# Kernel optimization log

Hardware: AMD Instinct MI355X
Metric: run time of the kernel (lower is better)

## Reference

```python
import jax, jax.numpy as jnp
import numpy as np

FILTERS = 128
DN = ('NHWC', 'HWIO', 'NHWC')
T1 = 1.0
RTOL = 1e-3
ATOL = 1e-3
DT0 = 0.05
MAX_STEPS = 32  # upper bound on adaptive solver steps (dopri5 at rtol=1e-3 uses far fewer)


def _conv(x, w):
    return jax.lax.conv_general_dilated(x, w, (1, 1), 'SAME', dimension_numbers=DN)


def _ode_func(y, t, w1, b1, w2, b2):
    # f(y, t) = relu(conv(relu(conv([y, t], w1)+b1) ++ t, w2)+b2), time appended as extra channel
    def cat_t(x):
        return jnp.concatenate([x, jnp.ones(x.shape[:-1] + (1,), x.dtype) * t], axis=-1)
    h = jax.nn.relu(_conv(cat_t(y), w1) + b1)
    return jax.nn.relu(_conv(cat_t(h), w2) + b2)


def _dopri5(y0, w1, b1, w2, b2):
    # Adaptive Dormand-Prince RK45 from t=0 to t=1, matching tf.contrib.integrate.odeint defaults
    f = lambda y, t: _ode_func(y, t, w1, b1, w2, b2)

    def rk_step(y, t, dt):
        k1 = f(y, t)
        k2 = f(y + dt * (0.2 * k1), t + 0.2 * dt)
        k3 = f(y + dt * (3. / 40 * k1 + 9. / 40 * k2), t + 0.3 * dt)
        k4 = f(y + dt * (44. / 45 * k1 - 56. / 15 * k2 + 32. / 9 * k3), t + 0.8 * dt)
        k5 = f(y + dt * (19372. / 6561 * k1 - 25360. / 2187 * k2 + 64448. / 6561 * k3
                         - 212. / 729 * k4), t + 8. / 9 * dt)
        k6 = f(y + dt * (9017. / 3168 * k1 - 355. / 33 * k2 + 46732. / 5247 * k3
                         + 49. / 176 * k4 - 5103. / 18656 * k5), t + dt)
        y5 = y + dt * (35. / 384 * k1 + 500. / 1113 * k3 + 125. / 192 * k4
                       - 2187. / 6784 * k5 + 11. / 84 * k6)
        k7 = f(y5, t + dt)  # FSAL stage, used only for the error estimate here
        err = dt * ((35. / 384 - 5179. / 57600) * k1 + (500. / 1113 - 7571. / 16695) * k3
                    + (125. / 192 - 393. / 640) * k4 + (-2187. / 6784 + 92097. / 339200) * k5
                    + (11. / 84 - 187. / 2100) * k6 - (1. / 40) * k7)
        return y5, err

    def step(carry, _):
        y, t, dt, done = carry
        dt_c = jnp.minimum(dt, T1 - t)  # never overshoot t1
        y_new, err = rk_step(y, t, dt_c)
        scale = ATOL + RTOL * jnp.maximum(jnp.abs(y), jnp.abs(y_new))
        err_norm = jnp.sqrt(jnp.mean(jnp.square(err / scale)))
        err_norm = jax.lax.stop_gradient(jnp.maximum(err_norm, 1e-10))
        accept = err_norm <= 1.0
        factor = jnp.clip(0.9 * err_norm ** -0.2, 0.2, 10.0)
        adv = accept & jnp.logical_not(done)
        y = jnp.where(adv, y_new, y)
        t = jnp.where(adv, t + dt_c, t)
        dt = jnp.where(done, dt, dt_c * factor)
        done = done | (t >= T1 - 1e-6)
        return (y, t, dt, done), None

    init = (y0, jnp.float32(0.0), jnp.float32(DT0), jnp.array(False))
    (y, _, _, _), _ = jax.lax.scan(jax.checkpoint(step), init, None, length=MAX_STEPS)
    return y


def setup_inputs() -> dict:
    key = jax.random.key(0)
    k0, k1, k2 = jax.random.split(key, 3)
    B, H, W, F = 32, 32, 32, FILTERS
    kh = kw = 3
    # glorot_uniform for HWIO conv kernel: fan_in = kh*kw*(F+1), fan_out = kh*kw*F
    lim = float(np.sqrt(6.0 / (kh * kw * (F + 1) + kh * kw * F)))
    x = jax.random.normal(k0, (B, H, W, F), jnp.float32)
    w1 = jax.random.uniform(k1, (kh, kw, F + 1, F), jnp.float32, -lim, lim)
    w2 = jax.random.uniform(k2, (kh, kw, F + 1, F), jnp.float32, -lim, lim)
    b1 = jnp.zeros((F,), jnp.float32)
    b2 = jnp.zeros((F,), jnp.float32)
    return {"x": x, "w1": w1, "b1": b1, "w2": w2, "b2": b2}


def reference(x, w1, b1, w2, b2):
    return _dopri5(x, w1, b1, w2, b2)
```

## Files before the change

kernel.cpp:

```cpp
#include <hip/hip_runtime.h>
#include <math.h>

#define NB    32
#define NHW   32
#define NC    128
#define NTOT  (NB*NHW*NHW*NC)
#define N4    (NTOT/4)
#define N8    (NTOT/8)
#define KDIM  1152

typedef unsigned short u16;
typedef __attribute__((ext_vector_type(8))) short short8v;
typedef __attribute__((ext_vector_type(4))) float float4v;

__device__ inline float b2f(u16 u) { union { unsigned int i; float f; } x; x.i = ((unsigned int)u) << 16; return x.f; }
__device__ inline u16   f2b(float f) {
    union { unsigned int i; float f; } x; x.f = f;
    unsigned int u = x.i;
    return (u16)((u + 0x7fffu + ((u >> 16) & 1u)) >> 16);
}
__device__ inline void ld8(const u16* __restrict__ p, float* v) {
    uint4 r = *(const uint4*)p;
    v[0] = b2f((u16)(r.x & 0xffff)); v[1] = b2f((u16)(r.x >> 16));
    v[2] = b2f((u16)(r.y & 0xffff)); v[3] = b2f((u16)(r.y >> 16));
    v[4] = b2f((u16)(r.z & 0xffff)); v[5] = b2f((u16)(r.z >> 16));
    v[6] = b2f((u16)(r.w & 0xffff)); v[7] = b2f((u16)(r.w >> 16));
}
__device__ inline uint4 pk8(const float* v) {
    uint4 o;
    o.x = (unsigned int)f2b(v[0]) | ((unsigned int)f2b(v[1]) << 16);
    o.y = (unsigned int)f2b(v[2]) | ((unsigned int)f2b(v[3]) << 16);
    o.z = (unsigned int)f2b(v[4]) | ((unsigned int)f2b(v[5]) << 16);
    o.w = (unsigned int)f2b(v[6]) | ((unsigned int)f2b(v[7]) << 16);
    return o;
}
__device__ inline void fma8(float* __restrict__ v, const u16* __restrict__ p, float s) {
    float kv[8];
    ld8(p, kv);
    #pragma unroll
    for (int j = 0; j < 8; ++j) v[j] = fmaf(s, kv[j], v[j]);
}


__global__ __launch_bounds__(64) void init_kernel(float* __restrict__ st, double* __restrict__ acc)
{
    int i = threadIdx.x;
    if (i < 32) acc[i] = 0.0;
    if (i == 0) { st[0]=0.0f; st[1]=0.05f; st[2]=0.05f; st[3]=0.0f; st[4]=0.0f; }
}

__global__ __launch_bounds__(256) void prep_kernel(
    const float* __restrict__ w, short* __restrict__ Wt, float* __restrict__ Et)
{
    const int part = blockIdx.x;
    const int tid = threadIdx.x;
    if (part < 9) {
        const int tap = part;
        for (int i = tid; i < 128*128; i += 256) {
            const int ci = i >> 7, co = i & 127;
            Wt[co*KDIM + tap*128 + ci] = (short)f2b(w[(tap*129 + ci)*128 + co]);
        }
    } else {
        for (int i = tid; i < 9*128; i += 256) {
            const int cls = i >> 7, co = i & 127;
            const int cy = cls / 3, cx = cls % 3;
            float s = 0.f;
            for (int ky = 0; ky < 3; ++ky) {
                if ((cy==0 && ky==0) || (cy==2 && ky==2)) continue;
                for (int kx = 0; kx < 3; ++kx) {
                    if ((cx==0 && kx==0) || (cx==2 && kx==2)) continue;
                    s += w[((ky*3+kx)*129 + 128)*128 + co];
                }
            }
            Et[cls*128 + co] = s;
        }
    }
}

__global__ __launch_bounds__(256) void copy_kernel(float* __restrict__ dst, const float* __restrict__ src)
{
    int stride = gridDim.x * blockDim.x;
    for (int i = blockIdx.x*blockDim.x + threadIdx.x; i < N4; i += stride)
        reinterpret_cast<float4*>(dst)[i] = reinterpret_cast<const float4*>(src)[i];
}

__global__ __launch_bounds__(256) void copy_if_adv_kernel(float* __restrict__ dst,
                                                          const float* __restrict__ src,
                                                          const float* __restrict__ st)
{
    if (st[4] == 0.0f) return;
    int stride = gridDim.x * blockDim.x;
    for (int i = blockIdx.x*blockDim.x + threadIdx.x; i < N4; i += stride)
        reinterpret_cast<float4*>(dst)[i] = reinterpret_cast<const float4*>(src)[i];
}

template<int NK>
__global__ __launch_bounds__(256) void conv_mfma(
    const float* __restrict__ basef, const u16* __restrict__ bfin,
    const u16* __restrict__ ka, const u16* __restrict__ kb,
    const u16* __restrict__ kc, const u16* __restrict__ kd,
    const u16* __restrict__ ke,
    float ca, float cb, float cc2, float cd, float ce,
    const short* __restrict__ Wt, const float* __restrict__ bias,
    const float* __restrict__ Et,
    u16* __restrict__ out,
    const float* __restrict__ st, float cfrac)
{
    if (st[3] != 0.0f) return;
    __shared__ __align__(16) char lds[180*256];
    const int b    = blockIdx.y;
    const int tile = blockIdx.x;
    const int ty   = (tile >> 2) * 16;
    const int tx   = (tile & 3) * 8;
    const int tid  = threadIdx.x;
    const float dt = st[2];

    const size_t ibase = (size_t)b * (NHW*NHW*NC);
    for (int i = tid; i < 180*16; i += 256) {
        const int pos = i >> 4, cc = i & 15;
        const int sy = pos / 10, sx = pos - sy*10;
        const int gy = ty + sy - 1, gx = tx + sx - 1;
        const bool ok = ((unsigned)gy < 32u) && ((unsigned)gx < 32u);
        uint4 w128;
        if (!ok) {
            w128 = make_uint4(0u, 0u, 0u, 0u);
        } else if (NK < 0) {
            w128 = *(const uint4*)(bfin + ibase + (size_t)(gy*32 + gx)*128 + cc*8);
        } else {
            const size_t idx = ibase + (size_t)(gy*32 + gx)*128 + cc*8;
            float v[8];
            *(float4*)(v)     = *(const float4*)(basef + idx);
            *(float4*)(v + 4) = *(const float4*)(basef + idx + 4);
            if (NK >= 1) fma8(v, ka + idx, dt*ca);
            if (NK >= 2) fma8(v, kb + idx, dt*cb);
            if (NK >= 3) fma8(v, kc + idx, dt*cc2);
            if (NK >= 4) fma8(v, kd + idx, dt*cd);
            if (NK >= 5) fma8(v, ke + idx, dt*ce);
            w128 = pk8(v);
        }
        *(uint4*)(lds + pos*256 + ((cc*16) ^ ((pos & 7) << 4))) = w128;
    }
    __syncthreads();

    const int l  = tid & 63;
    const int w  = tid >> 6;
    const int wy = w >> 1, wx = w & 1;
    const int lr = l & 15,  kg = l >> 4;

    float4v acc[4][4];
    #pragma unroll
    for (int ra = 0; ra < 4; ++ra)
        #pragma unroll
        for (int nb = 0; nb < 4; ++nb)
            acc[ra][nb] = (float4v){0.f, 0.f, 0.f, 0.f};

    int sy0[4], sx0[4];
    #pragma unroll
    for (int ra = 0; ra < 4; ++ra) {
        const int r = wy*64 + ra*16 + lr;
        sy0[ra] = r >> 3; sx0[ra] = r & 7;
    }

    #pragma unroll
    for (int ky = 0; ky < 3; ++ky) {
        #pragma unroll
        for (int kx = 0; kx < 3; ++kx) {
            const int tap = ky*3 + kx;
            #pragma unroll
            for (int kk = 0; kk < 4; ++kk) {
                short8v a[4], bb[4];
                const int cc = kk*4 + kg;
                #pragma unroll
                for (int ra = 0; ra < 4; ++ra) {
                    const int pos = (sy0[ra] + ky)*10 + sx0[ra] + kx;
                    a[ra] = *(const short8v*)(lds + pos*256 + ((cc*16) ^ ((pos & 7) << 4)));
                }
                const short* wb = Wt + tap*128 + kk*32 + kg*8;
                #pragma unroll
                for (int nb = 0; nb < 4; ++nb) {
                    const int cout = wx*64 + nb*16 + lr;
                    bb[nb] = *(const short8v*)(wb + (size_t)cout*KDIM);
                }
                #pragma unroll
                for (int ra = 0; ra < 4; ++ra)
                    #pragma unroll
                    for (int nb = 0; nb < 4; ++nb)
                        acc[ra][nb] = __builtin_amdgcn_mfma_f32_16x16x32_bf16(a[ra], bb[nb], acc[ra][nb], 0, 0, 0);
            }
        }
    }

    const float tval = st[0] + cfrac*dt;
    #pragma unroll
    for (int nb = 0; nb < 4; ++nb) {
        const int cout = wx*64 + nb*16 + lr;
        const float bsv = bias[cout];
        #pragma unroll
        for (int ra = 0; ra < 4; ++ra) {
            #pragma unroll
            for (int ri = 0; ri < 4; ++ri) {
                const int r  = wy*64 + ra*16 + kg*4 + ri;
                const int yy = ty + (r >> 3), xx = tx + (r & 7);
                const int cy = (yy == 0) ? 0 : ((yy == 31) ? 2 : 1);
                const int cx = (xx == 0) ? 0 : ((xx == 31) ? 2 : 1);
                float v = acc[ra][nb][ri] + bsv + tval*Et[(cy*3 + cx)*128 + cout];
                v = fmaxf(v, 0.f);
                out[(size_t)b*131072 + (size_t)(yy*32 + xx)*128 + cout] = f2b(v);
            }
        }
    }
}

__global__ __launch_bounds__(256) void axpy5_kernel(
    float* __restrict__ y5, const float* __restrict__ y,
    const u16* __restrict__ k1, const u16* __restrict__ k3,
    const u16* __restrict__ k4, const u16* __restrict__ k5,
    const u16* __restrict__ k6,
    float c1, float c3, float c4, float c5, float c6,
    const float* __restrict__ st)
{
    if (st[3] != 0.0f) return;
    const float dt = st[2];
    int stride = gridDim.x * blockDim.x;
    for (int i = blockIdx.x*blockDim.x + threadIdx.x; i < N8; i += stride) {
        const size_t base = (size_t)i * 8;
        float v[8];
        *(float4*)(v)     = *(const float4*)(y + base);
        *(float4*)(v + 4) = *(const float4*)(y + base + 4);
        fma8(v, k1 + base, dt*c1);
        fma8(v, k3 + base, dt*c3);
        fma8(v, k4 + base, dt*c4);
        fma8(v, k5 + base, dt*c5);
        fma8(v, k6 + base, dt*c6);
        *(float4*)(y5 + base)     = *(const float4*)(v);
        *(float4*)(y5 + base + 4) = *(const float4*)(v + 4);
    }
}

__global__ __launch_bounds__(256) void err_reduce_kernel(
    const float* __restrict__ y,  const float* __restrict__ y5,
    const u16* __restrict__ k1, const u16* __restrict__ k3,
    const u16* __restrict__ k4, const u16* __restrict__ k5,
    const u16* __restrict__ k6, const u16* __restrict__ k7,
    const float* __restrict__ st, double* __restrict__ acc_slot)
{
    if (st[3] != 0.0f) return;
    const float dt = st[2];
    const float E1 = (float)(35.0/384.0 - 5179.0/57600.0);
    const float E3 = (float)(500.0/1113.0 - 7571.0/16695.0);
    const float E4 = (float)(125.0/192.0 - 393.0/640.0);
    const float E5 = (float)(-2187.0/6784.0 + 92097.0/339200.0);
    const float E6 = (float)(11.0/84.0 - 187.0/2100.0);
    const float E7 = (float)(-1.0/40.0);
    float lsum = 0.f;
    int stride = gridDim.x*blockDim.x;
    for (int i = blockIdx.x*blockDim.x + threadIdx.x; i < N8; i += stride) {
        const size_t base = (size_t)i * 8;
        float a[8], c[8], d[8], e[8], f[8], g[8], yv[8], v5[8];
        ld8(k1 + base, a); ld8(k3 + base, c); ld8(k4 + base, d);
        ld8(k5 + base, e); ld8(k6 + base, f); ld8(k7 + base, g);
        *(float4*)(yv)     = *(const float4*)(y + base);
        *(float4*)(yv + 4) = *(const float4*)(y + base + 4);
        *(float4*)(v5)     = *(const float4*)(y5 + base);
        *(float4*)(v5 + 4) = *(const float4*)(y5 + base + 4);
        #pragma unroll
        for (int j = 0; j < 8; ++j) {
            float err = dt*(E1*a[j] + E3*c[j] + E4*d[j] + E5*e[j] + E6*f[j] + E7*g[j]);
            float sc  = 1e-3f + 1e-3f*fmaxf(fabsf(yv[j]), fabsf(v5[j]));
            float r = err/sc; lsum += r*r;
        }
    }
    #pragma unroll
    for (int off = 32; off > 0; off >>= 1) lsum += __shfl_down(lsum, off, 64);
    __shared__ float ws_[4];
    int wid = threadIdx.x >> 6, lane = threadIdx.x & 63;
    if (lane == 0) ws_[wid] = lsum;
    __syncthreads();
    if (threadIdx.x == 0) {
        float bs = ws_[0] + ws_[1] + ws_[2] + ws_[3];
        atomicAdd(acc_slot, (double)bs);
    }
}

__global__ __launch_bounds__(64) void ctrl_kernel(float* __restrict__ st, const double* __restrict__ acc_slot)
{
    if (threadIdx.x != 0) return;
    float t = st[0], dt = st[1], dtc = st[2];
    bool done = (st[3] != 0.0f);
    float err_norm = sqrtf((float)(*acc_slot / (double)NTOT));
    err_norm = fmaxf(err_norm, 1e-10f);
    bool accept = (err_norm <= 1.0f);
    float factor = 0.9f * powf(err_norm, -0.2f);
    factor = fminf(fmaxf(factor, 0.2f), 10.0f);
    bool adv = accept && !done;
    if (adv) t = t + dtc;
    if (!done) dt = dtc * factor;
    done = done || (t >= 1.0f - 1e-6f);
    st[0] = t; st[1] = dt; st[3] = done ? 1.0f : 0.0f; st[4] = adv ? 1.0f : 0.0f;
    st[2] = fminf(dt, 1.0f - t);
}

extern "C" void kernel_launch(void* const* d_in, const int* in_sizes, int n_in,
                              void* d_out, int out_size, void* d_ws, size_t ws_size,
                              hipStream_t stream)
{
    const float* x  = (const float*)d_in[0];
    const float* w1 = (const float*)d_in[1];
    const float* b1 = (const float*)d_in[2];
    const float* w2 = (const float*)d_in[3];
    const float* b2 = (const float*)d_in[4];

    char* ws = (char*)d_ws;
    double* acc = (double*)ws;
    float*  st  = (float*)(ws + 256);
    float*  E1t = (float*)(ws + 512);
    float*  E2t = (float*)(ws + 5120);
    short*  Wt1 = (short*)(ws + 10240);
    short*  Wt2 = (short*)(ws + 10240 + 294912);
    char*   bufs = ws + 1048576;
    float* y  = (float*)(bufs);
    float* y5 = (float*)(bufs + (size_t)NTOT*4);
    u16*   h  = (u16*)(bufs + (size_t)NTOT*8);
    u16*   k1 = (u16*)(bufs + (size_t)NTOT*10);
    u16*   k2 = (u16*)(bufs + (size_t)NTOT*12);
    u16*   k3 = (u16*)(bufs + (size_t)NTOT*14);
    u16*   k4 = (u16*)(bufs + (size_t)NTOT*16);
    u16*   k5 = (u16*)(bufs + (size_t)NTOT*18);
    u16*   k6 = (u16*)(bufs + (size_t)NTOT*20);
    u16*   k7 = (u16*)(bufs + (size_t)NTOT*22);

    const dim3 cgrid(8, NB);
    const dim3 cblk(256);
    const int ab = 2048;

    const float A21 = 0.2f;
    const float A31 = (float)(3.0/40.0),      A32 = (float)(9.0/40.0);
    const float A41 = (float)(44.0/45.0),     A42 = (float)(-56.0/15.0),     A43 = (float)(32.0/9.0);
    const float A51 = (float)(19372.0/6561.0),A52 = (float)(-25360.0/2187.0),A53 = (float)(64448.0/6561.0), A54 = (float)(-212.0/729.0);
    const float A61 = (float)(9017.0/3168.0), A62 = (float)(-355.0/33.0),    A63 = (float)(46732.0/5247.0), A64 = (float)(49.0/176.0), A65 = (float)(-5103.0/18656.0);
    const float B1  = (float)(35.0/384.0),    B3  = (float)(500.0/1113.0),   B4  = (float)(125.0/192.0),    B5  = (float)(-2187.0/6784.0), B6 = (float)(11.0/84.0);
    const float C2 = 0.2f, C3 = 0.3f, C4 = 0.8f, C5 = (float)(8.0/9.0);

    init_kernel<<<1, 64, 0, stream>>>(st, acc);
    prep_kernel<<<10, 256, 0, stream>>>(w1, Wt1, E1t);
    prep_kernel<<<10, 256, 0, stream>>>(w2, Wt2, E2t);
    copy_kernel<<<ab, 256, 0, stream>>>(y, x);

    for (int it = 0; it < 32; ++it) {
        conv_mfma<0><<<cgrid, cblk, 0, stream>>>(y, h, k1,k1,k1,k1,k1, 0,0,0,0,0, Wt1, b1, E1t, h,  st, 0.0f);
        conv_mfma<-1><<<cgrid, cblk, 0, stream>>>(y, h, k1,k1,k1,k1,k1, 0,0,0,0,0, Wt2, b2, E2t, k1, st, 0.0f);
        conv_mfma<1><<<cgrid, cblk, 0, stream>>>(y, h, k1,k1,k1,k1,k1, A21,0,0,0,0, Wt1, b1, E1t, h,  st, C2);
        conv_mfma<-1><<<cgrid, cblk, 0, stream>>>(y, h, k1,k1,k1,k1,k1, 0,0,0,0,0, Wt2, b2, E2t, k2, st, C2);
        conv_mfma<2><<<cgrid, cblk, 0, stream>>>(y, h, k1,k2,k1,k1,k1, A31,A32,0,0,0, Wt1, b1, E1t, h,  st, C3);
        conv_mfma<-1><<<cgrid, cblk, 0, stream>>>(y, h, k1,k1,k1,k1,k1, 0,0,0,0,0, Wt2, b2, E2t, k3, st, C3);
        conv_mfma<3><<<cgrid, cblk, 0, stream>>>(y, h, k1,k2,k3,k1,k1, A41,A42,A43,0,0, Wt1, b1, E1t, h,  st, C4);
        conv_mfma<-1><<<cgrid, cblk, 0, stream>>>(y, h, k1,k1,k1,k1,k1, 0,0,0,0,0, Wt2, b2, E2t, k4, st, C4);
        conv_mfma<4><<<cgrid, cblk, 0, stream>>>(y, h, k1,k2,k3,k4,k1, A51,A52,A53,A54,0, Wt1, b1, E1t, h,  st, C5);
        conv_mfma<-1><<<cgrid, cblk, 0, stream>>>(y, h, k1,k1,k1,k1,k1, 0,0,0,0,0, Wt2, b2, E2t, k5, st, C5);
        conv_mfma<5><<<cgrid, cblk, 0, stream>>>(y, h, k1,k2,k3,k4,k5, A61,A62,A63,A64,A65, Wt1, b1, E1t, h,  st, 1.0f);
        conv_mfma<-1><<<cgrid, cblk, 0, stream>>>(y, h, k1,k1,k1,k1,k1, 0,0,0,0,0, Wt2, b2, E2t, k6, st, 1.0f);
        axpy5_kernel<<<ab, 256, 0, stream>>>(y5, y, k1, k3, k4, k5, k6, B1, B3, B4, B5, B6, st);
        conv_mfma<0><<<cgrid, cblk, 0, stream>>>(y5, h, k1,k1,k1,k1,k1, 0,0,0,0,0, Wt1, b1, E1t, h,  st, 1.0f);
        conv_mfma<-1><<<cgrid, cblk, 0, stream>>>(y5, h, k1,k1,k1,k1,k1, 0,0,0,0,0, Wt2, b2, E2t, k7, st, 1.0f);
        err_reduce_kernel<<<ab, 256, 0, stream>>>(y, y5, k1, k3, k4, k5, k6, k7, st, acc + it);
        ctrl_kernel<<<1, 64, 0, stream>>>(st, acc + it);
        copy_if_adv_kernel<<<ab, 256, 0, stream>>>(y, y5, st);
    }

    copy_kernel<<<ab, 256, 0, stream>>>((float*)d_out, y);

    (void)in_sizes; (void)n_in; (void)out_size; (void)ws_size;
}
```

Baseline: 3.021 ms.

## Fuse both convolutions per stage with halo recompute and ping-pong state buffers

Each ODE function evaluation now runs in one kernel: the first conv is computed on a 10x10 halo region into LDS, then the second conv reads it directly, so the bf16 intermediate h no longer goes through global memory. The y5 combination is folded into the stage-7 evaluation, the error reduction and step control are merged using a last-block atomic counter, and y/y5 swap roles via a flag instead of a conditional copy. The cost is redundant halo computation in the first conv (100 positions computed for 64 outputs), 8x8 tiles with more blocks, and fewer kernel launches per step.

```diff
diff --git a/kernel.cpp b/kernel.cpp
--- a/kernel.cpp
+++ b/kernel.cpp
@@ -1,13 +1,11 @@
 #include <hip/hip_runtime.h>
 #include <math.h>
 
-#define NB    32
-#define NHW   32
-#define NC    128
-#define NTOT  (NB*NHW*NHW*NC)
-#define N4    (NTOT/4)
-#define N8    (NTOT/8)
+#define NTOT  4194304
+#define N4    1048576
+#define N8    524288
 #define KDIM  1152
+#define EGRID 512
 
 typedef unsigned short u16;
 typedef __attribute__((ext_vector_type(8))) short short8v;
@@ -41,12 +39,22 @@
     for (int j = 0; j < 8; ++j) v[j] = fmaf(s, kv[j], v[j]);
 }
 
-
-__global__ __launch_bounds__(64) void init_kernel(float* __restrict__ st, double* __restrict__ acc)
+constexpr float A21 = 0.2f;
+constexpr float A31 = (float)(3.0/40.0),       A32 = (float)(9.0/40.0);
+constexpr float A41 = (float)(44.0/45.0),      A42 = (float)(-56.0/15.0),      A43 = (float)(32.0/9.0);
+constexpr float A51 = (float)(19372.0/6561.0), A52 = (float)(-25360.0/2187.0), A53 = (float)(64448.0/6561.0), A54 = (float)(-212.0/729.0);
+constexpr float A61 = (float)(9017.0/3168.0),  A62 = (float)(-355.0/33.0),     A63 = (float)(46732.0/5247.0), A64 = (float)(49.0/176.0), A65 = (float)(-5103.0/18656.0);
+constexpr float B1c = (float)(35.0/384.0),     B3c = (float)(500.0/1113.0),    B4c = (float)(125.0/192.0),    B5c = (float)(-2187.0/6784.0), B6c = (float)(11.0/84.0);
+constexpr float CF2 = 0.2f, CF3 = 0.3f, CF4 = 0.8f, CF5 = (float)(8.0/9.0);
+
+
+__global__ __launch_bounds__(64) void init_kernel(float* __restrict__ st,
+                                                  double* __restrict__ acc,
+                                                  unsigned* __restrict__ cnt)
 {
     int i = threadIdx.x;
-    if (i < 32) acc[i] = 0.0;
-    if (i == 0) { st[0]=0.0f; st[1]=0.05f; st[2]=0.05f; st[3]=0.0f; st[4]=0.0f; }
+    if (i < 32) { acc[i] = 0.0; cnt[i] = 0u; }
+    if (i == 0) { st[0]=0.0f; st[1]=0.05f; st[2]=0.05f; st[3]=0.0f; st[4]=0.0f; st[5]=0.0f; }
 }
 
 __global__ __launch_bounds__(256) void prep_kernel(
@@ -77,183 +85,213 @@
     }
 }
 
-__global__ __launch_bounds__(256) void copy_kernel(float* __restrict__ dst, const float* __restrict__ src)
+__global__ __launch_bounds__(256) void copy_in_kernel(float* __restrict__ dst, const float* __restrict__ src)
 {
     int stride = gridDim.x * blockDim.x;
     for (int i = blockIdx.x*blockDim.x + threadIdx.x; i < N4; i += stride)
         reinterpret_cast<float4*>(dst)[i] = reinterpret_cast<const float4*>(src)[i];
 }
 
-__global__ __launch_bounds__(256) void copy_if_adv_kernel(float* __restrict__ dst,
-                                                          const float* __restrict__ src,
-                                                          const float* __restrict__ st)
-{
-    if (st[4] == 0.0f) return;
+__global__ __launch_bounds__(256) void copy_out_kernel(float* __restrict__ dst,
+                                                       const float* __restrict__ yA,
+                                                       const float* __restrict__ yB,
+                                                       const float* __restrict__ st)
+{
+    const float* y = (st[5] != 0.0f) ? yB : yA;
     int stride = gridDim.x * blockDim.x;
     for (int i = blockIdx.x*blockDim.x + threadIdx.x; i < N4; i += stride)
-        reinterpret_cast<float4*>(dst)[i] = reinterpret_cast<const float4*>(src)[i];
-}
-
-template<int NK>
-__global__ __launch_bounds__(256) void conv_mfma(
-    const float* __restrict__ basef, const u16* __restrict__ bfin,
+        reinterpret_cast<float4*>(dst)[i] = reinterpret_cast<const float4*>(y)[i];
+}
+
+template<int NK, bool STY5>
+__global__ __launch_bounds__(256) void feval_kernel(
+    const float* __restrict__ yAp, float* __restrict__ yBp,
     const u16* __restrict__ ka, const u16* __restrict__ kb,
     const u16* __restrict__ kc, const u16* __restrict__ kd,
     const u16* __restrict__ ke,
-    float ca, float cb, float cc2, float cd, float ce,
-    const short* __restrict__ Wt, const float* __restrict__ bias,
-    const float* __restrict__ Et,
-    u16* __restrict__ out,
+    float ca, float cb, float cc, float cd, float ce,
+    const short* __restrict__ Wt1, const float* __restrict__ b1g, const float* __restrict__ E1g,
+    const short* __restrict__ Wt2, const float* __restrict__ b2g, const float* __restrict__ E2g,
+    u16* __restrict__ kout,
     const float* __restrict__ st, float cfrac)
 {
     if (st[3] != 0.0f) return;
-    __shared__ __align__(16) char lds[180*256];
-    const int b    = blockIdx.y;
+    __shared__ __align__(16) char ldsA[144*256];
+    __shared__ __align__(16) char ldsH[100*256];
+
+    const int flag = (st[5] != 0.0f);
+    const float* yb  = flag ? (const float*)yBp : yAp;
+    float*       y5b = flag ? (float*)yAp : yBp;
+
+    const int img  = blockIdx.y;
     const int tile = blockIdx.x;
-    const int ty   = (tile >> 2) * 16;
+    const int ty   = ((tile >> 2) & 3) * 8;
     const int tx   = (tile & 3) * 8;
     const int tid  = threadIdx.x;
-    const float dt = st[2];
-
-    const size_t ibase = (size_t)b * (NHW*NHW*NC);
-    for (int i = tid; i < 180*16; i += 256) {
-        const int pos = i >> 4, cc = i & 15;
-        const int sy = pos / 10, sx = pos - sy*10;
-        const int gy = ty + sy - 1, gx = tx + sx - 1;
-        const bool ok = ((unsigned)gy < 32u) && ((unsigned)gx < 32u);
-        uint4 w128;
-        if (!ok) {
-            w128 = make_uint4(0u, 0u, 0u, 0u);
-        } else if (NK < 0) {
-            w128 = *(const uint4*)(bfin + ibase + (size_t)(gy*32 + gx)*128 + cc*8);
-        } else {
-            const size_t idx = ibase + (size_t)(gy*32 + gx)*128 + cc*8;
-            float v[8];
-            *(float4*)(v)     = *(const float4*)(basef + idx);
-            *(float4*)(v + 4) = *(const float4*)(basef + idx + 4);
-            if (NK >= 1) fma8(v, ka + idx, dt*ca);
-            if (NK >= 2) fma8(v, kb + idx, dt*cb);
-            if (NK >= 3) fma8(v, kc + idx, dt*cc2);
-            if (NK >= 4) fma8(v, kd + idx, dt*cd);
-            if (NK >= 5) fma8(v, ke + idx, dt*ce);
-            w128 = pk8(v);
-        }
-        *(uint4*)(lds + pos*256 + ((cc*16) ^ ((pos & 7) << 4))) = w128;
+    const float dt   = st[2];
+    const float tval = st[0] + cfrac * dt;
+    const size_t ibase = (size_t)img * 131072;
+
+    {
+        const float s1 = dt*ca, s2 = dt*cb, s3 = dt*cc, s4 = dt*cd, s5 = dt*ce;
+        for (int i = tid; i < 144*16; i += 256) {
+            const int pos = i >> 4, ch8 = i & 15;
+            const int iy = pos / 12, ix = pos - iy*12;
+            const int gy = ty + iy - 2, gx = tx + ix - 2;
+            uint4 w128 = make_uint4(0u, 0u, 0u, 0u);
+            if ((unsigned)gy < 32u && (unsigned)gx < 32u) {
+                const size_t idx = ibase + (size_t)((gy << 5) + gx)*128 + ch8*8;
+                float v[8];
+                *(float4*)(v)     = *(const float4*)(yb + idx);
+                *(float4*)(v + 4) = *(const float4*)(yb + idx + 4);
+                if (NK >= 1) fma8(v, ka + idx, s1);
+                if (NK >= 2) fma8(v, kb + idx, s2);
+                if (NK >= 3) fma8(v, kc + idx, s3);
+                if (NK >= 4) fma8(v, kd + idx, s4);
+                if (NK >= 5) fma8(v, ke + idx, s5);
+                if (STY5) {
+                    if ((unsigned)(iy - 2) < 8u && (unsigned)(ix - 2) < 8u) {
+                        *(float4*)(y5b + idx)     = *(const float4*)(v);
+                        *(float4*)(y5b + idx + 4) = *(const float4*)(v + 4);
+                    }
+                }
+                w128 = pk8(v);
+            }
+            *(uint4*)(ldsA + pos*256 + ((ch8*16) ^ ((pos & 7) << 4))) = w128;
+        }
     }
     __syncthreads();
 
-    const int l  = tid & 63;
-    const int w  = tid >> 6;
-    const int wy = w >> 1, wx = w & 1;
+    const int l  = tid & 63, w = tid >> 6;
     const int lr = l & 15,  kg = l >> 4;
 
-    float4v acc[4][4];
-    #pragma unroll
-    for (int ra = 0; ra < 4; ++ra)
-        #pragma unroll
-        for (int nb = 0; nb < 4; ++nb)
-            acc[ra][nb] = (float4v){0.f, 0.f, 0.f, 0.f};
-
-    int sy0[4], sx0[4];
-    #pragma unroll
-    for (int ra = 0; ra < 4; ++ra) {
-        const int r = wy*64 + ra*16 + lr;
-        sy0[ra] = r >> 3; sx0[ra] = r & 7;
-    }
-
-    #pragma unroll
-    for (int ky = 0; ky < 3; ++ky) {
-        #pragma unroll
-        for (int kx = 0; kx < 3; ++kx) {
-            const int tap = ky*3 + kx;
+    {
+        float4v acc[2][8];
+        #pragma unroll
+        for (int j = 0; j < 2; ++j)
             #pragma unroll
-            for (int kk = 0; kk < 4; ++kk) {
-                short8v a[4], bb[4];
-                const int cc = kk*4 + kg;
+            for (int cf = 0; cf < 8; ++cf) acc[j][cf] = (float4v){0.f, 0.f, 0.f, 0.f};
+        int py[2], px[2];
+        #pragma unroll
+        for (int j = 0; j < 2; ++j) {
+            const int p = (w*2 + j)*16 + lr;
+            py[j] = p / 10; px[j] = p - py[j]*10;
+        }
+        #pragma unroll 1
+        for (int ky = 0; ky < 3; ++ky) {
+            #pragma unroll 1
+            for (int kx = 0; kx < 3; ++kx) {
+                const int tap = ky*3 + kx;
                 #pragma unroll
-                for (int ra = 0; ra < 4; ++ra) {
-                    const int pos = (sy0[ra] + ky)*10 + sx0[ra] + kx;
-                    a[ra] = *(const short8v*)(lds + pos*256 + ((cc*16) ^ ((pos & 7) << 4)));
+                for (int kk = 0; kk < 4; ++kk) {
+                    short8v a[2], bb[8];
+                    #pragma unroll
+                    for (int j = 0; j < 2; ++j) {
+                        int pp = (py[j] + ky)*12 + px[j] + kx;
+                        pp = (pp < 144) ? pp : 143;
+                        a[j] = *(const short8v*)(ldsA + pp*256 + ((16*(kk*4 + kg)) ^ ((pp & 7) << 4)));
+                    }
+                    const short* wb = Wt1 + tap*128 + kk*32 + kg*8;
+                    #pragma unroll
+                    for (int cf = 0; cf < 8; ++cf)
+                        bb[cf] = *(const short8v*)(wb + (size_t)(cf*16 + lr)*KDIM);
+                    #pragma unroll
+                    for (int j = 0; j < 2; ++j)
+                        #pragma unroll
+                        for (int cf = 0; cf < 8; ++cf)
+                            acc[j][cf] = __builtin_amdgcn_mfma_f32_16x16x32_bf16(a[j], bb[cf], acc[j][cf], 0, 0, 0);
                 }
-                const short* wb = Wt + tap*128 + kk*32 + kg*8;
-                #pragma unroll
-                for (int nb = 0; nb < 4; ++nb) {
-                    const int cout = wx*64 + nb*16 + lr;
-                    bb[nb] = *(const short8v*)(wb + (size_t)cout*KDIM);
-                }
-                #pragma unroll
-                for (int ra = 0; ra < 4; ++ra)
-                    #pragma unroll
-                    for (int nb = 0; nb < 4; ++nb)
-                        acc[ra][nb] = __builtin_amdgcn_mfma_f32_16x16x32_bf16(a[ra], bb[nb], acc[ra][nb], 0, 0, 0);
-            }
-        }
-    }
-
-    const float tval = st[0] + cfrac*dt;
-    #pragma unroll
-    for (int nb = 0; nb < 4; ++nb) {
-        const int cout = wx*64 + nb*16 + lr;
-        const float bsv = bias[cout];
-        #pragma unroll
-        for (int ra = 0; ra < 4; ++ra) {
+            }
+        }
+        #pragma unroll
+        for (int j = 0; j < 2; ++j)
             #pragma unroll
             for (int ri = 0; ri < 4; ++ri) {
-                const int r  = wy*64 + ra*16 + kg*4 + ri;
-                const int yy = ty + (r >> 3), xx = tx + (r & 7);
-                const int cy = (yy == 0) ? 0 : ((yy == 31) ? 2 : 1);
-                const int cx = (xx == 0) ? 0 : ((xx == 31) ? 2 : 1);
-                float v = acc[ra][nb][ri] + bsv + tval*Et[(cy*3 + cx)*128 + cout];
-                v = fmaxf(v, 0.f);
-                out[(size_t)b*131072 + (size_t)(yy*32 + xx)*128 + cout] = f2b(v);
-            }
-        }
-    }
-}
-
-__global__ __launch_bounds__(256) void axpy5_kernel(
-    float* __restrict__ y5, const float* __restrict__ y,
-    const u16* __restrict__ k1, const u16* __restrict__ k3,
-    const u16* __restrict__ k4, const u16* __restrict__ k5,
-    const u16* __restrict__ k6,
-    float c1, float c3, float c4, float c5, float c6,
-    const float* __restrict__ st)
-{
-    if (st[3] != 0.0f) return;
-    const float dt = st[2];
-    int stride = gridDim.x * blockDim.x;
-    for (int i = blockIdx.x*blockDim.x + threadIdx.x; i < N8; i += stride) {
-        const size_t base = (size_t)i * 8;
-        float v[8];
-        *(float4*)(v)     = *(const float4*)(y + base);
-        *(float4*)(v + 4) = *(const float4*)(y + base + 4);
-        fma8(v, k1 + base, dt*c1);
-        fma8(v, k3 + base, dt*c3);
-        fma8(v, k4 + base, dt*c4);
-        fma8(v, k5 + base, dt*c5);
-        fma8(v, k6 + base, dt*c6);
-        *(float4*)(y5 + base)     = *(const float4*)(v);
-        *(float4*)(y5 + base + 4) = *(const float4*)(v + 4);
-    }
-}
-
-__global__ __launch_bounds__(256) void err_reduce_kernel(
-    const float* __restrict__ y,  const float* __restrict__ y5,
+                const int p = (w*2 + j)*16 + kg*4 + ri;
+                if (p < 100) {
+                    const int hy = p / 10, hx = p - (p/10)*10;
+                    const int gy = ty + hy - 1, gx = tx + hx - 1;
+                    const bool in = ((unsigned)gy < 32u) && ((unsigned)gx < 32u);
+                    const int cy = (gy == 0) ? 0 : ((gy == 31) ? 2 : 1);
+                    const int cx = (gx == 0) ? 0 : ((gx == 31) ? 2 : 1);
+                    const int ecl = (cy*3 + cx)*128;
+                    #pragma unroll
+                    for (int cf = 0; cf < 8; ++cf) {
+                        const int c = cf*16 + lr;
+                        float v = 0.f;
+                        if (in) v = fmaxf(acc[j][cf][ri] + b1g[c] + tval*E1g[ecl + c], 0.f);
+                        *(u16*)(ldsH + p*256 + ((2*c) ^ ((p & 7) << 4))) = f2b(v);
+                    }
+                }
+            }
+    }
+    __syncthreads();
+
+    {
+        float4v acc[8];
+        #pragma unroll
+        for (int cf = 0; cf < 8; ++cf) acc[cf] = (float4v){0.f, 0.f, 0.f, 0.f};
+        const int r = w*16 + lr;
+        const int oy = r >> 3, ox = r & 7;
+        #pragma unroll 1
+        for (int ky = 0; ky < 3; ++ky) {
+            #pragma unroll 1
+            for (int kx = 0; kx < 3; ++kx) {
+                const int tap = ky*3 + kx;
+                #pragma unroll
+                for (int kk = 0; kk < 4; ++kk) {
+                    const int p = (oy + ky)*10 + ox + kx;
+                    short8v a = *(const short8v*)(ldsH + p*256 + ((16*(kk*4 + kg)) ^ ((p & 7) << 4)));
+                    const short* wb = Wt2 + tap*128 + kk*32 + kg*8;
+                    short8v bb[8];
+                    #pragma unroll
+                    for (int cf = 0; cf < 8; ++cf)
+                        bb[cf] = *(const short8v*)(wb + (size_t)(cf*16 + lr)*KDIM);
+                    #pragma unroll
+                    for (int cf = 0; cf < 8; ++cf)
+                        acc[cf] = __builtin_amdgcn_mfma_f32_16x16x32_bf16(a, bb[cf], acc[cf], 0, 0, 0);
+                }
+            }
+        }
+        #pragma unroll
+        for (int ri = 0; ri < 4; ++ri) {
+            const int r2  = w*16 + kg*4 + ri;
+            const int gy  = ty + (r2 >> 3), gx = tx + (r2 & 7);
+            const int cy  = (gy == 0) ? 0 : ((gy == 31) ? 2 : 1);
+            const int cx  = (gx == 0) ? 0 : ((gx == 31) ? 2 : 1);
+            const int ecl = (cy*3 + cx)*128;
+            const size_t obase = ibase + (size_t)((gy << 5) + gx)*128;
+            #pragma unroll
+            for (int cf = 0; cf < 8; ++cf) {
+                const int c = cf*16 + lr;
+                float v = fmaxf(acc[cf][ri] + b2g[c] + tval*E2g[ecl + c], 0.f);
+                kout[obase + c] = f2b(v);
+            }
+        }
+    }
+}
+
+__global__ __launch_bounds__(256) void err_ctrl_kernel(
+    const float* __restrict__ yAp, const float* __restrict__ yBp,
     const u16* __restrict__ k1, const u16* __restrict__ k3,
     const u16* __restrict__ k4, const u16* __restrict__ k5,
     const u16* __restrict__ k6, const u16* __restrict__ k7,
-    const float* __restrict__ st, double* __restrict__ acc_slot)
+    float* __restrict__ st, double* __restrict__ acc, unsigned* __restrict__ cnt,
+    int it)
 {
     if (st[3] != 0.0f) return;
+    const int flag = (st[5] != 0.0f);
+    const float* y  = flag ? yBp : yAp;
+    const float* y5 = flag ? yAp : yBp;
     const float dt = st[2];
-    const float E1 = (float)(35.0/384.0 - 5179.0/57600.0);
-    const float E3 = (float)(500.0/1113.0 - 7571.0/16695.0);
-    const float E4 = (float)(125.0/192.0 - 393.0/640.0);
-    const float E5 = (float)(-2187.0/6784.0 + 92097.0/339200.0);
-    const float E6 = (float)(11.0/84.0 - 187.0/2100.0);
-    const float E7 = (float)(-1.0/40.0);
+    const float ER1 = (float)(35.0/384.0 - 5179.0/57600.0);
+    const float ER3 = (float)(500.0/1113.0 - 7571.0/16695.0);
+    const float ER4 = (float)(125.0/192.0 - 393.0/640.0);
+    const float ER5 = (float)(-2187.0/6784.0 + 92097.0/339200.0);
+    const float ER6 = (float)(11.0/84.0 - 187.0/2100.0);
+    const float ER7 = (float)(-1.0/40.0);
     float lsum = 0.f;
-    int stride = gridDim.x*blockDim.x;
+    const int stride = gridDim.x * blockDim.x;
     for (int i = blockIdx.x*blockDim.x + threadIdx.x; i < N8; i += stride) {
         const size_t base = (size_t)i * 8;
         float a[8], c[8], d[8], e[8], f[8], g[8], yv[8], v5[8];
@@ -265,109 +303,102 @@
         *(float4*)(v5 + 4) = *(const float4*)(y5 + base + 4);
         #pragma unroll
         for (int j = 0; j < 8; ++j) {
-            float err = dt*(E1*a[j] + E3*c[j] + E4*d[j] + E5*e[j] + E6*f[j] + E7*g[j]);
+            float err = dt*(ER1*a[j] + ER3*c[j] + ER4*d[j] + ER5*e[j] + ER6*f[j] + ER7*g[j]);
             float sc  = 1e-3f + 1e-3f*fmaxf(fabsf(yv[j]), fabsf(v5[j]));
-            float r = err/sc; lsum += r*r;
+            float rr = err/sc; lsum += rr*rr;
         }
     }
     #pragma unroll
     for (int off = 32; off > 0; off >>= 1) lsum += __shfl_down(lsum, off, 64);
     __shared__ float ws_[4];
-    int wid = threadIdx.x >> 6, lane = threadIdx.x & 63;
+    const int wid = threadIdx.x >> 6, lane = threadIdx.x & 63;
     if (lane == 0) ws_[wid] = lsum;
     __syncthreads();
     if (threadIdx.x == 0) {
-        float bs = ws_[0] + ws_[1] + ws_[2] + ws_[3];
-        atomicAdd(acc_slot, (double)bs);
-    }
-}
-
-__global__ __launch_bounds__(64) void ctrl_kernel(float* __restrict__ st, const double* __restrict__ acc_slot)
-{
-    if (threadIdx.x != 0) return;
-    float t = st[0], dt = st[1], dtc = st[2];
-    bool done = (st[3] != 0.0f);
-    float err_norm = sqrtf((float)(*acc_slot / (double)NTOT));
-    err_norm = fmaxf(err_norm, 1e-10f);
-    bool accept = (err_norm <= 1.0f);
-    float factor = 0.9f * powf(err_norm, -0.2f);
-    factor = fminf(fmaxf(factor, 0.2f), 10.0f);
-    bool adv = accept && !done;
-    if (adv) t = t + dtc;
-    if (!done) dt = dtc * factor;
-    done = done || (t >= 1.0f - 1e-6f);
-    st[0] = t; st[1] = dt; st[3] = done ? 1.0f : 0.0f; st[4] = adv ? 1.0f : 0.0f;
-    st[2] = fminf(dt, 1.0f - t);
-}
+        const float bs = ws_[0] + ws_[1] + ws_[2] + ws_[3];
+        atomicAdd(acc + it, (double)bs);
+        __threadfence();
+        const unsigned v = atomicAdd(cnt + it, 1u);
+        if (v == (unsigned)(EGRID - 1)) {
+            __threadfence();
+            const double a = atomicAdd(acc + it, 0.0);
+            float t = st[0], dtp = st[1], dtc = st[2];
+            float en = sqrtf((float)(a / (double)NTOT));
+            en = fmaxf(en, 1e-10f);
+            const bool accept = (en <= 1.0f);
+            float factor = fminf(fmaxf(0.9f * powf(en, -0.2f), 0.2f), 10.0f);
+            const bool adv = accept;
+            if (adv) t += dtc;
+            dtp = dtc * factor;
+            const bool done = (t >= 1.0f - 1e-6f);
+            st[0] = t; st[1] = dtp;
+            st[2] = fminf(dtp, 1.0f - t);
+            st[3] = done ? 1.0f : 0.0f;
+            st[4] = adv ? 1.0f : 0.0f;
+            if (adv) st[5] = flag ? 0.0f : 1.0f;
+        }
+    }
+}
+
 
 extern "C" void kernel_launch(void* const* d_in, const int* in_sizes, int n_in,
                               void* d_out, int out_size, void* d_ws, size_t ws_size,
                               hipStream_t stream)
 {
-    const float* x  = (const float*)d_in[0];
-    const float* w1 = (const float*)d_in[1];
-    const float* b1 = (const float*)d_in[2];
-    const float* w2 = (const float*)d_in[3];
-    const float* b2 = (const float*)d_in[4];
-
-    char* ws = (char*)d_ws;
-    double* acc = (double*)ws;
-    float*  st  = (float*)(ws + 256);
-    float*  E1t = (float*)(ws + 512);
-    float*  E2t = (float*)(ws + 5120);
-    short*  Wt1 = (short*)(ws + 10240);
-    short*  Wt2 = (short*)(ws + 10240 + 294912);
-    char*   bufs = ws + 1048576;
-    float* y  = (float*)(bufs);
-    float* y5 = (float*)(bufs + (size_t)NTOT*4);
-    u16*   h  = (u16*)(bufs + (size_t)NTOT*8);
-    u16*   k1 = (u16*)(bufs + (size_t)NTOT*10);
-    u16*   k2 = (u16*)(bufs + (size_t)NTOT*12);
-    u16*   k3 = (u16*)(bufs + (size_t)NTOT*14);
-    u16*   k4 = (u16*)(bufs + (size_t)NTOT*16);
-    u16*   k5 = (u16*)(bufs + (size_t)NTOT*18);
-    u16*   k6 = (u16*)(bufs + (size_t)NTOT*20);
-    u16*   k7 = (u16*)(bufs + (size_t)NTOT*22);
-
-    const dim3 cgrid(8, NB);
-    const dim3 cblk(256);
-    const int ab = 2048;
-
-    const float A21 = 0.2f;
-    const float A31 = (float)(3.0/40.0),      A32 = (float)(9.0/40.0);
-    const float A41 = (float)(44.0/45.0),     A42 = (float)(-56.0/15.0),     A43 = (float)(32.0/9.0);
-    const float A51 = (float)(19372.0/6561.0),A52 = (float)(-25360.0/2187.0),A53 = (float)(64448.0/6561.0), A54 = (float)(-212.0/729.0);
-    const float A61 = (float)(9017.0/3168.0), A62 = (float)(-355.0/33.0),    A63 = (float)(46732.0/5247.0), A64 = (float)(49.0/176.0), A65 = (float)(-5103.0/18656.0);
-    const float B1  = (float)(35.0/384.0),    B3  = (float)(500.0/1113.0),   B4  = (float)(125.0/192.0),    B5  = (float)(-2187.0/6784.0), B6 = (float)(11.0/84.0);
-    const float C2 = 0.2f, C3 = 0.3f, C4 = 0.8f, C5 = (float)(8.0/9.0);
-
-    init_kernel<<<1, 64, 0, stream>>>(st, acc);
-    prep_kernel<<<10, 256, 0, stream>>>(w1, Wt1, E1t);
-    prep_kernel<<<10, 256, 0, stream>>>(w2, Wt2, E2t);
-    copy_kernel<<<ab, 256, 0, stream>>>(y, x);
+    const float* xp  = (const float*)d_in[0];
+    const float* w1p = (const float*)d_in[1];
+    const float* b1p = (const float*)d_in[2];
+    const float* w2p = (const float*)d_in[3];
+    const float* b2p = (const float*)d_in[4];
+    char*  wsp  = (char*)d_ws;
+    float* outp = (float*)d_out;
+
+    double*   acc = (double*)wsp;
+    unsigned* cnt = (unsigned*)(wsp + 256);
+    float*    st  = (float*)(wsp + 512);
+    float*    E1t = (float*)(wsp + 1024);
+    float*    E2t = (float*)(wsp + 5632);
+    short*    Wt1 = (short*)(wsp + 10240);
+    short*    Wt2 = (short*)(wsp + 305152);
+    char*     bufs = wsp + 1048576;
+    float* yA = (float*)(bufs);
+    float* yB = (float*)(bufs + (size_t)NTOT*4);
+    u16* k1 = (u16*)(bufs + (size_t)NTOT*8);
+    u16* k2 = (u16*)(bufs + (size_t)NTOT*10);
+    u16* k3 = (u16*)(bufs + (size_t)NTOT*12);
+    u16* k4 = (u16*)(bufs + (size_t)NTOT*14);
+    u16* k5 = (u16*)(bufs + (size_t)NTOT*16);
+    u16* k6 = (u16*)(bufs + (size_t)NTOT*18);
+    u16* k7 = (u16*)(bufs + (size_t)NTOT*20);
+
+    const dim3 fgrid(16, 32);
+    const dim3 fblk(256);
+
+    init_kernel<<<1, 64, 0, stream>>>(st, acc, cnt);
+    prep_kernel<<<10, 256, 0, stream>>>(w1p, Wt1, E1t);
+    prep_kernel<<<10, 256, 0, stream>>>(w2p, Wt2, E2t);
+    copy_in_kernel<<<2048, 256, 0, stream>>>(yA, xp);
 
     for (int it = 0; it < 32; ++it) {
-        conv_mfma<0><<<cgrid, cblk, 0, stream>>>(y, h, k1,k1,k1,k1,k1, 0,0,0,0,0, Wt1, b1, E1t, h,  st, 0.0f);
-        conv_mfma<-1><<<cgrid, cblk, 0, stream>>>(y, h, k1,k1,k1,k1,k1, 0,0,0,0,0, Wt2, b2, E2t, k1, st, 0.0f);
-        conv_mfma<1><<<cgrid, cblk, 0, stream>>>(y, h, k1,k1,k1,k1,k1, A21,0,0,0,0, Wt1, b1, E1t, h,  st, C2);
-        conv_mfma<-1><<<cgrid, cblk, 0, stream>>>(y, h, k1,k1,k1,k1,k1, 0,0,0,0,0, Wt2, b2, E2t, k2, st, C2);
-        conv_mfma<2><<<cgrid, cblk, 0, stream>>>(y, h, k1,k2,k1,k1,k1, A31,A32,0,0,0, Wt1, b1, E1t, h,  st, C3);
-        conv_mfma<-1><<<cgrid, cblk, 0, stream>>>(y, h, k1,k1,k1,k1,k1, 0,0,0,0,0, Wt2, b2, E2t, k3, st, C3);
-        conv_mfma<3><<<cgrid, cblk, 0, stream>>>(y, h, k1,k2,k3,k1,k1, A41,A42,A43,0,0, Wt1, b1, E1t, h,  st, C4);
-        conv_mfma<-1><<<cgrid, cblk, 0, stream>>>(y, h, k1,k1,k1,k1,k1, 0,0,0,0,0, Wt2, b2, E2t, k4, st, C4);
-        conv_mfma<4><<<cgrid, cblk, 0, stream>>>(y, h, k1,k2,k3,k4,k1, A51,A52,A53,A54,0, Wt1, b1, E1t, h,  st, C5);
-        conv_mfma<-1><<<cgrid, cblk, 0, stream>>>(y, h, k1,k1,k1,k1,k1, 0,0,0,0,0, Wt2, b2, E2t, k5, st, C5);
-        conv_mfma<5><<<cgrid, cblk, 0, stream>>>(y, h, k1,k2,k3,k4,k5, A61,A62,A63,A64,A65, Wt1, b1, E1t, h,  st, 1.0f);
-        conv_mfma<-1><<<cgrid, cblk, 0, stream>>>(y, h, k1,k1,k1,k1,k1, 0,0,0,0,0, Wt2, b2, E2t, k6, st, 1.0f);
-        axpy5_kernel<<<ab, 256, 0, stream>>>(y5, y, k1, k3, k4, k5, k6, B1, B3, B4, B5, B6, st);
-        conv_mfma<0><<<cgrid, cblk, 0, stream>>>(y5, h, k1,k1,k1,k1,k1, 0,0,0,0,0, Wt1, b1, E1t, h,  st, 1.0f);
-        conv_mfma<-1><<<cgrid, cblk, 0, stream>>>(y5, h, k1,k1,k1,k1,k1, 0,0,0,0,0, Wt2, b2, E2t, k7, st, 1.0f);
-        err_reduce_kernel<<<ab, 256, 0, stream>>>(y, y5, k1, k3, k4, k5, k6, k7, st, acc + it);
-        ctrl_kernel<<<1, 64, 0, stream>>>(st, acc + it);
-        copy_if_adv_kernel<<<ab, 256, 0, stream>>>(y, y5, st);
-    }
-
-    copy_kernel<<<ab, 256, 0, stream>>>((float*)d_out, y);
+        feval_kernel<0,false><<<fgrid, fblk, 0, stream>>>(yA, yB, k1,k1,k1,k1,k1, 0,0,0,0,0,
+            Wt1,b1p,E1t, Wt2,b2p,E2t, k1, st, 0.0f);
+        feval_kernel<1,false><<<fgrid, fblk, 0, stream>>>(yA, yB, k1,k1,k1,k1,k1, A21,0,0,0,0,
+            Wt1,b1p,E1t, Wt2,b2p,E2t, k2, st, CF2);
+        feval_kernel<2,false><<<fgrid, fblk, 0, stream>>>(yA, yB, k1,k2,k2,k2,k2, A31,A32,0,0,0,
+            Wt1,b1p,E1t, Wt2,b2p,E2t, k3, st, CF3);
+        feval_kernel<3,false><<<fgrid, fblk, 0, stream>>>(yA, yB, k1,k2,k3,k3,k3, A41,A42,A43,0,0,
+            Wt1,b1p,E1t, Wt2,b2p,E2t, k4, st, CF4);
+        feval_kernel<4,false><<<fgrid, fblk, 0, stream>>>(yA, yB, k1,k2,k3,k4,k4, A51,A52,A53,A54,0,
+            Wt1,b1p,E1t, Wt2,b2p,E2t, k5, st, CF5);
+        feval_kernel<5,false><<<fgrid, fblk, 0, stream>>>(yA, yB, k1,k2,k3,k4,k5, A61,A62,A63,A64,A65,
+            Wt1,b1p,E1t, Wt2,b2p,E2t, k6, st, 1.0f);
+        feval_kernel<5,true><<<fgrid, fblk, 0, stream>>>(yA, yB, k1,k3,k4,k5,k6, B1c,B3c,B4c,B5c,B6c,
+            Wt1,b1p,E1t, Wt2,b2p,E2t, k7, st, 1.0f);
+        err_ctrl_kernel<<<EGRID, 256, 0, stream>>>(yA, yB, k1, k3, k4, k5, k6, k7,
+            st, acc, cnt, it);
+    }
+
+    copy_out_kernel<<<2048, 256, 0, stream>>>(outp, yA, yB, st);
 
     (void)in_sizes; (void)n_in; (void)out_size; (void)ws_size;
 }
```

Measured after the change: 4.604 ms. 52.4% more time.
